# Kernel tuning notes

Measured on AMD Instinct MI355X. Metric: run time of the kernel, lower is better.

Reference implementation:

```python
import jax, jax.numpy as jnp
import numpy as np

B, T, I, H, O = 256, 512, 128, 512, 64
ALPHA = 0.2          # cfg.leak
BETA = 8.0           # cfg.softplus_beta
THRESH = 20.0        # cfg.softplus_threshold


def _phi(x):
    # F.softplus(x, beta, threshold): linear when beta*x > threshold
    z = BETA * x
    return jnp.where(z > THRESH, x, jax.nn.softplus(jnp.minimum(z, THRESH)) / BETA)


def setup_inputs() -> dict:
    key = jax.random.key(0)
    ks = jax.random.split(key, 6)
    x = jax.random.normal(ks[0], (B, T, I), dtype=jnp.float32)
    W_xh = jax.random.normal(ks[1], (H, I), dtype=jnp.float32) * (1.0 / np.sqrt(I))
    # E/I structure: column-wise sign (abs weights * sign), scaled to modest spectral radius
    sign = np.ones(H, dtype=np.float32)
    perm = np.random.default_rng(0).permutation(H)
    sign[perm[int(round(0.8 * H)):]] = -1.0
    W_hh = jnp.abs(jax.random.normal(ks[2], (H, H), dtype=jnp.float32)) * jnp.asarray(sign)[None, :]
    W_hh = W_hh * (1.2 / (jnp.linalg.norm(W_hh, ord=2) + 1e-6))
    b_h = jnp.zeros((H,), dtype=jnp.float32)
    W_out = jax.random.normal(ks[3], (O, H), dtype=jnp.float32) * (1.0 / np.sqrt(H))
    b_out = jnp.zeros((O,), dtype=jnp.float32)
    return {"x": x, "W_xh": W_xh, "W_hh": W_hh, "b_h": b_h, "W_out": W_out, "b_out": b_out}


def reference(x, W_xh, W_hh, b_h, W_out, b_out):
    # precompute input projection: [B,T,H]
    xw = jnp.einsum('bti,hi->bth', x, W_xh)

    def step(h, xw_t):  # h: [B,H], xw_t: [B,H]
        pre = xw_t + h @ W_hh.T + b_h
        h = (1.0 - ALPHA) * h + ALPHA * _phi(pre)
        y = h @ W_out.T + b_out  # readout='all'
        return h, y

    h0 = jnp.zeros((x.shape[0], W_hh.shape[0]), dtype=x.dtype)
    _, ys = jax.lax.scan(step, h0, jnp.swapaxes(xw, 0, 1))  # ys: [T,B,O]
    return jnp.swapaxes(ys, 0, 1)  # [B,T,O]
```

## Files before the change

### kernel.cpp

```cpp
#include <hip/hip_runtime.h>


#define BB 256
#define TT 512
#define II 128
#define HH 512
#define OO 64
#define RG 16
#define JC 64
#define NG 16
#define NC 8

typedef _Float16 f16;
typedef f16 f16x8 __attribute__((ext_vector_type(8)));
typedef float f32x4 __attribute__((ext_vector_type(4)));

__global__ __launch_bounds__(256, 1)
void eirnn_persist(const float* __restrict__ x,
                   const float* __restrict__ Wxh,
                   const float* __restrict__ Whh,
                   const float* __restrict__ bh,
                   const float* __restrict__ Wout,
                   const float* __restrict__ bout,
                   float* __restrict__ yout,
                   f16* __restrict__ hbuf,
                   unsigned int* __restrict__ flg)
{
    const int tid  = threadIdx.x;
    const int bid  = blockIdx.x;
    const int wave = tid >> 6;
    const int lane = tid & 63;
    const int quad = lane >> 4;
    const int l16  = lane & 15;
    const int r    = bid >> 3;
    const int c    = bid & 7;
    const int rowbase = r * RG;
    const int jbase   = c * JC;
    const int myrow   = wave * 16 + l16;

    __shared__ __align__(16) f16 hg[RG][HH + 8];
    __shared__ __align__(16) f16 xsh[RG][II + 8];

    f16x8 bf[16];
    f16x8 xbf[4];
    f16x8 bfo[2];
    {
        const float* wp = Whh + (size_t)(jbase + myrow) * HH + quad * 8;
        #pragma unroll
        for (int ks = 0; ks < 16; ++ks) {
            float4 u = *(const float4*)(wp + ks * 32);
            float4 v = *(const float4*)(wp + ks * 32 + 4);
            f16x8 tv;
            tv[0]=(f16)u.x; tv[1]=(f16)u.y; tv[2]=(f16)u.z; tv[3]=(f16)u.w;
            tv[4]=(f16)v.x; tv[5]=(f16)v.y; tv[6]=(f16)v.z; tv[7]=(f16)v.w;
            bf[ks] = tv;
        }
        const float* wq = Wxh + (size_t)(jbase + myrow) * II + quad * 8;
        #pragma unroll
        for (int ks = 0; ks < 4; ++ks) {
            float4 u = *(const float4*)(wq + ks * 32);
            float4 v = *(const float4*)(wq + ks * 32 + 4);
            f16x8 tv;
            tv[0]=(f16)u.x; tv[1]=(f16)u.y; tv[2]=(f16)u.z; tv[3]=(f16)u.w;
            tv[4]=(f16)v.x; tv[5]=(f16)v.y; tv[6]=(f16)v.z; tv[7]=(f16)v.w;
            xbf[ks] = tv;
        }
        const float* wo = Wout + (size_t)myrow * HH + c * 64 + quad * 8;
        #pragma unroll
        for (int ks = 0; ks < 2; ++ks) {
            float4 u = *(const float4*)(wo + ks * 32);
            float4 v = *(const float4*)(wo + ks * 32 + 4);
            f16x8 tv;
            tv[0]=(f16)u.x; tv[1]=(f16)u.y; tv[2]=(f16)u.z; tv[3]=(f16)u.w;
            tv[4]=(f16)v.x; tv[5]=(f16)v.y; tv[6]=(f16)v.z; tv[7]=(f16)v.w;
            bfo[ks] = tv;
        }
    }
    const float biash = bh[jbase + myrow];
    const float biaso = (c == 0) ? bout[myrow] : 0.0f;

    for (int p = tid; p < RG * (HH + 8) / 2; p += 256)
        ((unsigned int*)hg)[p] = 0u;

    float hreg[4] = {0.f, 0.f, 0.f, 0.f};

    const int col8  = tid & 127;
    const int shard = col8 >> 4;
    const int pw    = (tid & 15) >> 2;
    const int row0  = tid >> 7;
    const unsigned int* fpoll = flg + ((r * NC + shard) * 4 + pw);
    unsigned int* fmine = flg + ((r * NC + c) * 4 + wave);

    float4 xpf0, xpf1;
    {
        int p0 = tid, p1 = tid + 256;
        xpf0 = ((const float4*)(x + ((size_t)(rowbase + (p0 >> 5)) * TT + 0) * II))[p0 & 31];
        xpf1 = ((const float4*)(x + ((size_t)(rowbase + (p1 >> 5)) * TT + 0) * II))[p1 & 31];
    }

    __syncthreads();

    for (int t = 0; t <= TT; ++t) {
        if (t < TT) {
            int p0 = tid, p1 = tid + 256;
            f16* d0 = &xsh[p0 >> 5][(p0 & 31) * 4];
            d0[0]=(f16)xpf0.x; d0[1]=(f16)xpf0.y; d0[2]=(f16)xpf0.z; d0[3]=(f16)xpf0.w;
            f16* d1 = &xsh[p1 >> 5][(p1 & 31) * 4];
            d1[0]=(f16)xpf1.x; d1[1]=(f16)xpf1.y; d1[2]=(f16)xpf1.z; d1[3]=(f16)xpf1.w;
        }
        if (t + 1 < TT) {
            int p0 = tid, p1 = tid + 256;
            xpf0 = ((const float4*)(x + ((size_t)(rowbase + (p0 >> 5)) * TT + (t + 1)) * II))[p0 & 31];
            xpf1 = ((const float4*)(x + ((size_t)(rowbase + (p1 >> 5)) * TT + (t + 1)) * II))[p1 & 31];
        }
        if (t >= 1) {
            while (__hip_atomic_load(fpoll, __ATOMIC_RELAXED, __HIP_MEMORY_SCOPE_AGENT)
                   < (unsigned)t) {}
            const unsigned long long* src = (const unsigned long long*)hbuf
                + (size_t)(t & 1) * (BB * HH / 4) + (size_t)rowbase * (HH / 4) + col8;
            unsigned long long v[8];
            #pragma unroll
            for (int i = 0; i < 8; ++i)
                v[i] = __hip_atomic_load(src + (size_t)(row0 + 2 * i) * (HH / 4),
                                         __ATOMIC_RELAXED, __HIP_MEMORY_SCOPE_AGENT);
            #pragma unroll
            for (int i = 0; i < 8; ++i)
                *(unsigned long long*)&hg[row0 + 2 * i][col8 * 4] = v[i];
        }
        __syncthreads();

        if (t < TT) {
            f32x4 acc0 = {0.f,0.f,0.f,0.f}, acc1 = {0.f,0.f,0.f,0.f};
            #pragma unroll
            for (int ks = 0; ks < 16; ks += 2) {
                f16x8 a0 = *(const f16x8*)&hg[l16][ks * 32 + quad * 8];
                f16x8 a1 = *(const f16x8*)&hg[l16][(ks + 1) * 32 + quad * 8];
                acc0 = __builtin_amdgcn_mfma_f32_16x16x32_f16(a0, bf[ks], acc0, 0, 0, 0);
                acc1 = __builtin_amdgcn_mfma_f32_16x16x32_f16(a1, bf[ks + 1], acc1, 0, 0, 0);
            }
            #pragma unroll
            for (int ks = 0; ks < 4; ks += 2) {
                f16x8 a0 = *(const f16x8*)&xsh[l16][ks * 32 + quad * 8];
                f16x8 a1 = *(const f16x8*)&xsh[l16][(ks + 1) * 32 + quad * 8];
                acc0 = __builtin_amdgcn_mfma_f32_16x16x32_f16(a0, xbf[ks], acc0, 0, 0, 0);
                acc1 = __builtin_amdgcn_mfma_f32_16x16x32_f16(a1, xbf[ks + 1], acc1, 0, 0, 0);
            }
            unsigned int* dstw = (unsigned int*)hbuf + (size_t)((t + 1) & 1) * (BB * HH / 2);
            unsigned int hb[4];
            #pragma unroll
            for (int reg = 0; reg < 4; ++reg) {
                float pre = acc0[reg] + acc1[reg] + biash;
                float z = 8.f * pre;
                float ph = (z > 20.f) ? pre : (__logf(1.f + __expf(z)) * 0.125f);
                float hn = 0.8f * hreg[reg] + 0.2f * ph;
                hreg[reg] = hn;
                hb[reg] = (unsigned int)__builtin_bit_cast(unsigned short, (f16)hn);
            }
            #pragma unroll
            for (int reg = 0; reg < 4; ++reg) {
                unsigned int ob = (unsigned int)__shfl_xor((int)hb[reg], 1, 64);
                if ((lane & 1) == 0) {
                    size_t eidx = (size_t)(rowbase + quad * 4 + reg) * HH + jbase + myrow;
                    __hip_atomic_store(dstw + (eidx >> 1), hb[reg] | (ob << 16),
                                       __ATOMIC_RELAXED, __HIP_MEMORY_SCOPE_AGENT);
                }
            }
            __builtin_amdgcn_s_waitcnt(0);
            if (lane == 0)
                __hip_atomic_store(fmine, (unsigned)(t + 1),
                                   __ATOMIC_RELAXED, __HIP_MEMORY_SCOPE_AGENT);
        }

        if (t >= 1) {
            f32x4 ya = {0.f,0.f,0.f,0.f};
            f16x8 a0 = *(const f16x8*)&hg[l16][c * 64 + quad * 8];
            f16x8 a1 = *(const f16x8*)&hg[l16][c * 64 + 32 + quad * 8];
            ya = __builtin_amdgcn_mfma_f32_16x16x32_f16(a0, bfo[0], ya, 0, 0, 0);
            ya = __builtin_amdgcn_mfma_f32_16x16x32_f16(a1, bfo[1], ya, 0, 0, 0);
            #pragma unroll
            for (int reg = 0; reg < 4; ++reg)
                atomicAdd(yout + ((size_t)(rowbase + quad * 4 + reg) * TT + (t - 1)) * OO + myrow,
                          ya[reg] + biaso);
        }
        __syncthreads();
    }
}

extern "C" void kernel_launch(void* const* d_in, const int* in_sizes, int n_in,
                              void* d_out, int out_size, void* d_ws, size_t ws_size,
                              hipStream_t stream)
{
    const float* x    = (const float*)d_in[0];
    const float* Wxh  = (const float*)d_in[1];
    const float* Whh  = (const float*)d_in[2];
    const float* bh   = (const float*)d_in[3];
    const float* Wout = (const float*)d_in[4];
    const float* bout = (const float*)d_in[5];
    float* yout = (float*)d_out;

    f16* hbuf = (f16*)d_ws;
    const size_t hbuf_bytes = (size_t)2 * BB * HH * sizeof(f16);
    unsigned int* flg = (unsigned int*)((char*)d_ws + hbuf_bytes);
    const size_t flg_bytes = (size_t)NG * NC * 4 * sizeof(unsigned int);

    if (ws_size < hbuf_bytes + flg_bytes) return;

    hipMemsetAsync(flg, 0, flg_bytes, stream);
    hipMemsetAsync(yout, 0, (size_t)out_size * sizeof(float), stream);

    eirnn_persist<<<dim3(NG * NC), dim3(256), 0, stream>>>(
        x, Wxh, Whh, bh, Wout, bout, yout, hbuf, flg);
}
```

Measured before the change: 1.502 ms.

## Replace flag polling with step-tagged hidden-state words and double-buffered LDS

Each 64-bit hidden-state word now carries the step number in its upper half, so consumers poll the data itself rather than a separate flag. This removes the waitcnt-plus-flag-store round trip on the producer side and the dependent load after the flag poll on the consumer side. The block writes its own shard directly into a double-buffered LDS copy and skips fetching it from global memory. Double-buffering hg and xsh also allows the trailing __syncthreads to be dropped. In exchange, global traffic per exchange doubles because of the tag bits, and the consumer spin loop now checks 16 loads per thread.

```diff
diff --git a/kernel.cpp b/kernel.cpp
--- a/kernel.cpp
+++ b/kernel.cpp
@@ -23,8 +23,7 @@
                    const float* __restrict__ Wout,
                    const float* __restrict__ bout,
                    float* __restrict__ yout,
-                   f16* __restrict__ hbuf,
-                   unsigned int* __restrict__ flg)
+                   unsigned long long* __restrict__ hbuf)
 {
     const int tid  = threadIdx.x;
     const int bid  = blockIdx.x;
@@ -38,8 +37,8 @@
     const int jbase   = c * JC;
     const int myrow   = wave * 16 + l16;
 
-    __shared__ __align__(16) f16 hg[RG][HH + 8];
-    __shared__ __align__(16) f16 xsh[RG][II + 8];
+    __shared__ __align__(16) f16 hg[2][RG][HH + 8];
+    __shared__ __align__(16) f16 xsh[2][RG][II + 8];
 
     f16x8 bf[16];
     f16x8 xbf[4];
@@ -79,17 +78,13 @@
     const float biash = bh[jbase + myrow];
     const float biaso = (c == 0) ? bout[myrow] : 0.0f;
 
-    for (int p = tid; p < RG * (HH + 8) / 2; p += 256)
+    for (int p = tid; p < RG * (HH + 8); p += 256)
         ((unsigned int*)hg)[p] = 0u;
 
     float hreg[4] = {0.f, 0.f, 0.f, 0.f};
 
-    const int col8  = tid & 127;
-    const int shard = col8 >> 4;
-    const int pw    = (tid & 15) >> 2;
-    const int row0  = tid >> 7;
-    const unsigned int* fpoll = flg + ((r * NC + shard) * 4 + pw);
-    unsigned int* fmine = flg + ((r * NC + c) * 4 + wave);
+    const int j8     = tid;
+    const int gshard = j8 >> 5;
 
     float4 xpf0, xpf1;
     {
@@ -101,11 +96,13 @@
     __syncthreads();
 
     for (int t = 0; t <= TT; ++t) {
+        const int pcur = t & 1;
+
         if (t < TT) {
             int p0 = tid, p1 = tid + 256;
-            f16* d0 = &xsh[p0 >> 5][(p0 & 31) * 4];
+            f16* d0 = &xsh[pcur][p0 >> 5][(p0 & 31) * 4];
             d0[0]=(f16)xpf0.x; d0[1]=(f16)xpf0.y; d0[2]=(f16)xpf0.z; d0[3]=(f16)xpf0.w;
-            f16* d1 = &xsh[p1 >> 5][(p1 & 31) * 4];
+            f16* d1 = &xsh[pcur][p1 >> 5][(p1 & 31) * 4];
             d1[0]=(f16)xpf1.x; d1[1]=(f16)xpf1.y; d1[2]=(f16)xpf1.z; d1[3]=(f16)xpf1.w;
         }
         if (t + 1 < TT) {
@@ -113,19 +110,31 @@
             xpf0 = ((const float4*)(x + ((size_t)(rowbase + (p0 >> 5)) * TT + (t + 1)) * II))[p0 & 31];
             xpf1 = ((const float4*)(x + ((size_t)(rowbase + (p1 >> 5)) * TT + (t + 1)) * II))[p1 & 31];
         }
-        if (t >= 1) {
-            while (__hip_atomic_load(fpoll, __ATOMIC_RELAXED, __HIP_MEMORY_SCOPE_AGENT)
-                   < (unsigned)t) {}
-            const unsigned long long* src = (const unsigned long long*)hbuf
-                + (size_t)(t & 1) * (BB * HH / 4) + (size_t)rowbase * (HH / 4) + col8;
-            unsigned long long v[8];
-            #pragma unroll
-            for (int i = 0; i < 8; ++i)
-                v[i] = __hip_atomic_load(src + (size_t)(row0 + 2 * i) * (HH / 4),
+        if (t >= 1 && gshard != c) {
+            const unsigned long long* src = hbuf
+                + (size_t)pcur * (BB * HH / 2)
+                + (size_t)rowbase * (HH / 2) + j8;
+            const unsigned int tg = (unsigned)t;
+            unsigned long long v[16];
+            #pragma unroll
+            for (int i = 0; i < 16; ++i)
+                v[i] = __hip_atomic_load(src + (size_t)i * (HH / 2),
                                          __ATOMIC_RELAXED, __HIP_MEMORY_SCOPE_AGENT);
-            #pragma unroll
-            for (int i = 0; i < 8; ++i)
-                *(unsigned long long*)&hg[row0 + 2 * i][col8 * 4] = v[i];
+            for (;;) {
+                bool any = false;
+                #pragma unroll
+                for (int i = 0; i < 16; ++i)
+                    any |= ((unsigned)(v[i] >> 32) != tg);
+                if (!any) break;
+                #pragma unroll
+                for (int i = 0; i < 16; ++i)
+                    if ((unsigned)(v[i] >> 32) != tg)
+                        v[i] = __hip_atomic_load(src + (size_t)i * (HH / 2),
+                                                 __ATOMIC_RELAXED, __HIP_MEMORY_SCOPE_AGENT);
+            }
+            #pragma unroll
+            for (int i = 0; i < 16; ++i)
+                *(unsigned int*)&hg[pcur][i][j8 * 2] = (unsigned int)v[i];
         }
         __syncthreads();
 
@@ -133,19 +142,20 @@
             f32x4 acc0 = {0.f,0.f,0.f,0.f}, acc1 = {0.f,0.f,0.f,0.f};
             #pragma unroll
             for (int ks = 0; ks < 16; ks += 2) {
-                f16x8 a0 = *(const f16x8*)&hg[l16][ks * 32 + quad * 8];
-                f16x8 a1 = *(const f16x8*)&hg[l16][(ks + 1) * 32 + quad * 8];
+                f16x8 a0 = *(const f16x8*)&hg[pcur][l16][ks * 32 + quad * 8];
+                f16x8 a1 = *(const f16x8*)&hg[pcur][l16][(ks + 1) * 32 + quad * 8];
                 acc0 = __builtin_amdgcn_mfma_f32_16x16x32_f16(a0, bf[ks], acc0, 0, 0, 0);
                 acc1 = __builtin_amdgcn_mfma_f32_16x16x32_f16(a1, bf[ks + 1], acc1, 0, 0, 0);
             }
             #pragma unroll
             for (int ks = 0; ks < 4; ks += 2) {
-                f16x8 a0 = *(const f16x8*)&xsh[l16][ks * 32 + quad * 8];
-                f16x8 a1 = *(const f16x8*)&xsh[l16][(ks + 1) * 32 + quad * 8];
+                f16x8 a0 = *(const f16x8*)&xsh[pcur][l16][ks * 32 + quad * 8];
+                f16x8 a1 = *(const f16x8*)&xsh[pcur][l16][(ks + 1) * 32 + quad * 8];
                 acc0 = __builtin_amdgcn_mfma_f32_16x16x32_f16(a0, xbf[ks], acc0, 0, 0, 0);
                 acc1 = __builtin_amdgcn_mfma_f32_16x16x32_f16(a1, xbf[ks + 1], acc1, 0, 0, 0);
             }
-            unsigned int* dstw = (unsigned int*)hbuf + (size_t)((t + 1) & 1) * (BB * HH / 2);
+            unsigned long long* dst64 = hbuf + (size_t)((t + 1) & 1) * (BB * HH / 2);
+            const unsigned long long tagw = ((unsigned long long)(unsigned)(t + 1)) << 32;
             unsigned int hb[4];
             #pragma unroll
             for (int reg = 0; reg < 4; ++reg) {
@@ -160,21 +170,19 @@
             for (int reg = 0; reg < 4; ++reg) {
                 unsigned int ob = (unsigned int)__shfl_xor((int)hb[reg], 1, 64);
                 if ((lane & 1) == 0) {
+                    unsigned int pair = hb[reg] | (ob << 16);
                     size_t eidx = (size_t)(rowbase + quad * 4 + reg) * HH + jbase + myrow;
-                    __hip_atomic_store(dstw + (eidx >> 1), hb[reg] | (ob << 16),
+                    __hip_atomic_store(dst64 + (eidx >> 1), tagw | (unsigned long long)pair,
                                        __ATOMIC_RELAXED, __HIP_MEMORY_SCOPE_AGENT);
+                    *(unsigned int*)&hg[(t + 1) & 1][quad * 4 + reg][jbase + myrow] = pair;
                 }
             }
-            __builtin_amdgcn_s_waitcnt(0);
-            if (lane == 0)
-                __hip_atomic_store(fmine, (unsigned)(t + 1),
-                                   __ATOMIC_RELAXED, __HIP_MEMORY_SCOPE_AGENT);
         }
 
         if (t >= 1) {
             f32x4 ya = {0.f,0.f,0.f,0.f};
-            f16x8 a0 = *(const f16x8*)&hg[l16][c * 64 + quad * 8];
-            f16x8 a1 = *(const f16x8*)&hg[l16][c * 64 + 32 + quad * 8];
+            f16x8 a0 = *(const f16x8*)&hg[pcur][l16][c * 64 + quad * 8];
+            f16x8 a1 = *(const f16x8*)&hg[pcur][l16][c * 64 + 32 + quad * 8];
             ya = __builtin_amdgcn_mfma_f32_16x16x32_f16(a0, bfo[0], ya, 0, 0, 0);
             ya = __builtin_amdgcn_mfma_f32_16x16x32_f16(a1, bfo[1], ya, 0, 0, 0);
             #pragma unroll
@@ -182,7 +190,6 @@
                 atomicAdd(yout + ((size_t)(rowbase + quad * 4 + reg) * TT + (t - 1)) * OO + myrow,
                           ya[reg] + biaso);
         }
-        __syncthreads();
     }
 }
 
@@ -198,16 +205,14 @@
     const float* bout = (const float*)d_in[5];
     float* yout = (float*)d_out;
 
-    f16* hbuf = (f16*)d_ws;
-    const size_t hbuf_bytes = (size_t)2 * BB * HH * sizeof(f16);
-    unsigned int* flg = (unsigned int*)((char*)d_ws + hbuf_bytes);
-    const size_t flg_bytes = (size_t)NG * NC * 4 * sizeof(unsigned int);
-
-    if (ws_size < hbuf_bytes + flg_bytes) return;
-
-    hipMemsetAsync(flg, 0, flg_bytes, stream);
+    unsigned long long* hbuf = (unsigned long long*)d_ws;
+    const size_t hbuf_bytes = (size_t)2 * BB * (HH / 2) * sizeof(unsigned long long);
+
+    if (ws_size < hbuf_bytes) return;
+
+    hipMemsetAsync(hbuf, 0, hbuf_bytes, stream);
     hipMemsetAsync(yout, 0, (size_t)out_size * sizeof(float), stream);
 
     eirnn_persist<<<dim3(NG * NC), dim3(256), 0, stream>>>(
-        x, Wxh, Whh, bh, Wout, bout, yout, hbuf, flg);
+        x, Wxh, Whh, bh, Wout, bout, yout, hbuf);
 }
```

Measured after the change: 1.396 ms. 1.08x faster.
